# Kernel optimization log

Hardware: AMD Instinct MI355X
Metric: run time of the kernel (lower is better)

Reference implementation:

```python
import jax, jax.numpy as jnp
import numpy as np

NUM_EMBEDDINGS = 1024
EMBEDDING_DIM = 64
BETA = 0.25


def setup_inputs() -> dict:
    key = jax.random.key(0)
    k1, k2 = jax.random.split(key)
    z = jax.random.normal(k1, (16, EMBEDDING_DIM, 64, 64), dtype=jnp.float32)
    # matches torch init: uniform_(-1/K, 1/K)
    lim = 1.0 / NUM_EMBEDDINGS
    embedding = jax.random.uniform(k2, (NUM_EMBEDDINGS, EMBEDDING_DIM),
                                   dtype=jnp.float32, minval=-lim, maxval=lim)
    return {"z": z, "embedding": embedding}


def reference(z, embedding):
    B, C, H, W = z.shape  # C == EMBEDDING_DIM
    # [B,C,H,W] -> [B*H*W, C]
    z_flat = jnp.transpose(z, (0, 2, 3, 1)).reshape(-1, C)
    # squared euclidean distances (argmin-equivalent to torch.cdist):
    # ||z||^2 - 2 z.e + ||e||^2 ; shape [N, K]
    d = (jnp.sum(z_flat * z_flat, axis=-1, keepdims=True)
         - 2.0 * (z_flat @ embedding.T)
         + jnp.sum(embedding * embedding, axis=-1))
    encoding_indices = jnp.argmin(d, axis=1)  # [N] int
    z_q_flat = embedding[encoding_indices]    # gather [N, C]
    z_q = jnp.transpose(z_q_flat.reshape(B, H, W, C), (0, 3, 1, 2))
    vq_loss = jnp.mean(jnp.square(jax.lax.stop_gradient(z_q) - z))
    commitment_loss = BETA * jnp.mean(jnp.square(jax.lax.stop_gradient(z) - z_q))
    return (z_q, encoding_indices, vq_loss + commitment_loss)
```

## Files before the change

kernel.cpp:

```cpp
#include <hip/hip_runtime.h>

#define N_PIX   65536
#define CDIM    64
#define KCODES  1024
#define HWSZ    4096
#define KCHUNK  128
#define NCHUNK  8
#define TPB     256
#define PXT     2

#define OFF_NE   0
#define OFF_MIN  1024
#define OFF_IDX  525312
#define OFF_LOSS 1049600

#define OUT_IDX  (N_PIX * CDIM)
#define OUT_LOSS (OUT_IDX + N_PIX)

__global__ void vq_prep(const float* __restrict__ emb, float* __restrict__ ws) {
#pragma clang fp contract(off)
    int k = blockIdx.x * blockDim.x + threadIdx.x;
    if (k == 0) ws[OFF_LOSS] = 0.0f;
    if (k >= KCODES) return;
    const float* e = emb + k * CDIM;
    float r0 = e[0]*e[0], r1 = e[1]*e[1], r2 = e[2]*e[2], r3 = e[3]*e[3];
    float r4 = e[4]*e[4], r5 = e[5]*e[5], r6 = e[6]*e[6], r7 = e[7]*e[7];
    for (int i = 8; i < CDIM; i += 8) {
        r0 = r0 + e[i+0]*e[i+0]; r1 = r1 + e[i+1]*e[i+1];
        r2 = r2 + e[i+2]*e[i+2]; r3 = r3 + e[i+3]*e[i+3];
        r4 = r4 + e[i+4]*e[i+4]; r5 = r5 + e[i+5]*e[i+5];
        r6 = r6 + e[i+6]*e[i+6]; r7 = r7 + e[i+7]*e[i+7];
    }
    ws[OFF_NE + k] = ((r0 + r1) + (r2 + r3)) + ((r4 + r5) + (r6 + r7));
}

__device__ __forceinline__ float np_nz(const float* zr) {
    float r0 = zr[0]*zr[0], r1 = zr[1]*zr[1], r2 = zr[2]*zr[2], r3 = zr[3]*zr[3];
    float r4 = zr[4]*zr[4], r5 = zr[5]*zr[5], r6 = zr[6]*zr[6], r7 = zr[7]*zr[7];
#pragma unroll
    for (int i = 8; i < CDIM; i += 8) {
        r0 = r0 + zr[i+0]*zr[i+0]; r1 = r1 + zr[i+1]*zr[i+1];
        r2 = r2 + zr[i+2]*zr[i+2]; r3 = r3 + zr[i+3]*zr[i+3];
        r4 = r4 + zr[i+4]*zr[i+4]; r5 = r5 + zr[i+5]*zr[i+5];
        r6 = r6 + zr[i+6]*zr[i+6]; r7 = r7 + zr[i+7]*zr[i+7];
    }
    return ((r0 + r1) + (r2 + r3)) + ((r4 + r5) + (r6 + r7));
}

__global__ __launch_bounds__(TPB, 2) void vq_argmin(const float* __restrict__ z,
                                                    const float* __restrict__ ws,
                                                    const float* __restrict__ emb,
                                                    float* __restrict__ cmin,
                                                    int* __restrict__ cidx) {
#pragma clang fp contract(off)
    __shared__ float se[KCHUNK * CDIM];
    __shared__ float sn[KCHUNK];

    const int chunk = blockIdx.y;
    const int k0 = chunk * KCHUNK;

    const float4* esrc = (const float4*)(emb + (size_t)k0 * CDIM);
    float4* edst = (float4*)se;
    for (int i = threadIdx.x; i < KCHUNK * CDIM / 4; i += TPB) edst[i] = esrc[i];
    for (int i = threadIdx.x; i < KCHUNK; i += TPB) sn[i] = ws[OFF_NE + k0 + i];
    __syncthreads();

    const int p0 = blockIdx.x * (TPB * PXT) + threadIdx.x;
    const int p1 = p0 + TPB;

    float zr0[CDIM], zr1[CDIM];
    {
        const int b0  = p0 >> 12, hw0 = p0 & (HWSZ - 1);
        const int b1  = p1 >> 12, hw1 = p1 & (HWSZ - 1);
        const float* zp0 = z + ((size_t)(b0 * CDIM) << 12) + hw0;
        const float* zp1 = z + ((size_t)(b1 * CDIM) << 12) + hw1;
#pragma unroll
        for (int c = 0; c < CDIM; ++c) {
            zr0[c] = zp0[(size_t)c << 12];
            zr1[c] = zp1[(size_t)c << 12];
        }
    }
    const float nz0 = np_nz(zr0);
    const float nz1 = np_nz(zr1);

    float best0 = 3.4e38f, best1 = 3.4e38f;
    int   bi0   = k0,      bi1   = k0;
    for (int kk = 0; kk < KCHUNK; kk += 2) {
        const float4* e0 = (const float4*)(se + kk * CDIM);
        const float4* e1 = e0 + (CDIM / 4);
        float a00 = 0.f, a01 = 0.f, a10 = 0.f, a11 = 0.f;
#pragma unroll
        for (int j = 0; j < 16; ++j) {
            float4 v0 = e0[j];
            float4 v1 = e1[j];
            a00 = fmaf(zr0[4*j+0], v0.x, a00);
            a00 = fmaf(zr0[4*j+1], v0.y, a00);
            a00 = fmaf(zr0[4*j+2], v0.z, a00);
            a00 = fmaf(zr0[4*j+3], v0.w, a00);
            a01 = fmaf(zr0[4*j+0], v1.x, a01);
            a01 = fmaf(zr0[4*j+1], v1.y, a01);
            a01 = fmaf(zr0[4*j+2], v1.z, a01);
            a01 = fmaf(zr0[4*j+3], v1.w, a01);
            a10 = fmaf(zr1[4*j+0], v0.x, a10);
            a10 = fmaf(zr1[4*j+1], v0.y, a10);
            a10 = fmaf(zr1[4*j+2], v0.z, a10);
            a10 = fmaf(zr1[4*j+3], v0.w, a10);
            a11 = fmaf(zr1[4*j+0], v1.x, a11);
            a11 = fmaf(zr1[4*j+1], v1.y, a11);
            a11 = fmaf(zr1[4*j+2], v1.z, a11);
            a11 = fmaf(zr1[4*j+3], v1.w, a11);
        }
        float d00 = (nz0 - 2.0f * a00) + sn[kk];
        float d01 = (nz0 - 2.0f * a01) + sn[kk + 1];
        float d10 = (nz1 - 2.0f * a10) + sn[kk];
        float d11 = (nz1 - 2.0f * a11) + sn[kk + 1];
        if (d00 < best0) { best0 = d00; bi0 = k0 + kk; }
        if (d01 < best0) { best0 = d01; bi0 = k0 + kk + 1; }
        if (d10 < best1) { best1 = d10; bi1 = k0 + kk; }
        if (d11 < best1) { best1 = d11; bi1 = k0 + kk + 1; }
    }
    cmin[(p0 << 3) + chunk] = best0;
    cidx[(p0 << 3) + chunk] = bi0;
    cmin[(p1 << 3) + chunk] = best1;
    cidx[(p1 << 3) + chunk] = bi1;
}

__global__ __launch_bounds__(TPB) void vq_finalize(const float* __restrict__ z,
                                                   const float* __restrict__ emb,
                                                   const float* __restrict__ cmin,
                                                   const int* __restrict__ cidx,
                                                   float* __restrict__ out,
                                                   float* __restrict__ loss_acc) {
    const int p = blockIdx.x * TPB + threadIdx.x;

    float best = cmin[p << 3];
    int   bi   = cidx[p << 3];
#pragma unroll
    for (int ch = 1; ch < NCHUNK; ++ch) {
        float m = cmin[(p << 3) + ch];
        if (m < best) { best = m; bi = cidx[(p << 3) + ch]; }
    }

    out[OUT_IDX + p] = (float)bi;

    const float* ev = emb + bi * CDIM;
    const int b  = p >> 12;
    const int hw = p & (HWSZ - 1);
    const float* zp = z + ((size_t)(b * CDIM) << 12) + hw;
    float* zq = out + ((size_t)(b * CDIM) << 12) + hw;

    float ls = 0.0f;
#pragma unroll
    for (int c = 0; c < CDIM; ++c) {
        float e = ev[c];
        float zv = zp[(size_t)c << 12];
        float d = e - zv;
        ls = fmaf(d, d, ls);
        zq[(size_t)c << 12] = e;
    }

#pragma unroll
    for (int off = 32; off > 0; off >>= 1) ls += __shfl_down(ls, off);
    __shared__ float wsum[TPB / 64];
    if ((threadIdx.x & 63) == 0) wsum[threadIdx.x >> 6] = ls;
    __syncthreads();
    if (threadIdx.x == 0) {
        float s = wsum[0] + wsum[1] + wsum[2] + wsum[3];
        atomicAdd(loss_acc, s);
    }
}

__global__ void vq_loss_out(const float* __restrict__ loss_acc, float* __restrict__ out) {
    out[OUT_LOSS] = loss_acc[0] * (1.25f / (float)(N_PIX * CDIM));
}

extern "C" void kernel_launch(void* const* d_in, const int* in_sizes, int n_in,
                              void* d_out, int out_size, void* d_ws, size_t ws_size,
                              hipStream_t stream) {
    const float* z   = (const float*)d_in[0];
    const float* emb = (const float*)d_in[1];
    float* ws   = (float*)d_ws;
    float* out  = (float*)d_out;
    float* cmin = ws + OFF_MIN;
    int*   cidx = (int*)(ws + OFF_IDX);
    float* lossp = ws + OFF_LOSS;

    vq_prep<<<dim3(KCODES / TPB), dim3(TPB), 0, stream>>>(emb, ws);
    vq_argmin<<<dim3(N_PIX / (TPB * PXT), NCHUNK), dim3(TPB), 0, stream>>>(z, ws, emb, cmin, cidx);
    vq_finalize<<<dim3(N_PIX / TPB), dim3(TPB), 0, stream>>>(z, emb, cmin, cidx, out, lossp);
    vq_loss_out<<<1, 1, 0, stream>>>(lossp, out);
}
```

Measured before the change: 197.2 us.

## Fuse prep and loss-out kernels, raise pixels per thread to four

Removes the separate codebook-norm prep kernel by computing norms in shared memory inside each argmin block. It also removes the final single-thread loss kernel by having the last finalize block, found through an atomic counter, write the scaled loss. Each thread now handles four pixels instead of two, halving the grid and doubling embedding reuse from shared memory, with launch bounds relaxed to one block per SIMD. The costs are much higher register pressure (256 z values per thread), which risks spills and lower occupancy, and fewer blocks (512) for the GPU's CUs.

Measured after the change: 304.3 us. +54.3%, slower.

```diff
diff --git a/kernel.cpp b/kernel.cpp
--- a/kernel.cpp
+++ b/kernel.cpp
@@ -7,32 +7,16 @@
 #define KCHUNK  128
 #define NCHUNK  8
 #define TPB     256
-#define PXT     2
-
-#define OFF_NE   0
+#define PXT     4
+#define GRIDX   (N_PIX / (TPB * PXT))
+
+#define OFF_CTR  0
 #define OFF_MIN  1024
 #define OFF_IDX  525312
 #define OFF_LOSS 1049600
 
 #define OUT_IDX  (N_PIX * CDIM)
 #define OUT_LOSS (OUT_IDX + N_PIX)
-
-__global__ void vq_prep(const float* __restrict__ emb, float* __restrict__ ws) {
-#pragma clang fp contract(off)
-    int k = blockIdx.x * blockDim.x + threadIdx.x;
-    if (k == 0) ws[OFF_LOSS] = 0.0f;
-    if (k >= KCODES) return;
-    const float* e = emb + k * CDIM;
-    float r0 = e[0]*e[0], r1 = e[1]*e[1], r2 = e[2]*e[2], r3 = e[3]*e[3];
-    float r4 = e[4]*e[4], r5 = e[5]*e[5], r6 = e[6]*e[6], r7 = e[7]*e[7];
-    for (int i = 8; i < CDIM; i += 8) {
-        r0 = r0 + e[i+0]*e[i+0]; r1 = r1 + e[i+1]*e[i+1];
-        r2 = r2 + e[i+2]*e[i+2]; r3 = r3 + e[i+3]*e[i+3];
-        r4 = r4 + e[i+4]*e[i+4]; r5 = r5 + e[i+5]*e[i+5];
-        r6 = r6 + e[i+6]*e[i+6]; r7 = r7 + e[i+7]*e[i+7];
-    }
-    ws[OFF_NE + k] = ((r0 + r1) + (r2 + r3)) + ((r4 + r5) + (r6 + r7));
-}
 
 __device__ __forceinline__ float np_nz(const float* zr) {
     float r0 = zr[0]*zr[0], r1 = zr[1]*zr[1], r2 = zr[2]*zr[2], r3 = zr[3]*zr[3];
@@ -47,11 +31,11 @@
     return ((r0 + r1) + (r2 + r3)) + ((r4 + r5) + (r6 + r7));
 }
 
-__global__ __launch_bounds__(TPB, 2) void vq_argmin(const float* __restrict__ z,
-                                                    const float* __restrict__ ws,
+__global__ __launch_bounds__(TPB, 1) void vq_argmin(const float* __restrict__ z,
                                                     const float* __restrict__ emb,
                                                     float* __restrict__ cmin,
-                                                    int* __restrict__ cidx) {
+                                                    int* __restrict__ cidx,
+                                                    float* __restrict__ ws) {
 #pragma clang fp contract(off)
     __shared__ float se[KCHUNK * CDIM];
     __shared__ float sn[KCHUNK];
@@ -59,36 +43,65 @@
     const int chunk = blockIdx.y;
     const int k0 = chunk * KCHUNK;
 
+    if ((blockIdx.x | blockIdx.y) == 0 && threadIdx.x == 0) {
+        ws[OFF_LOSS] = 0.0f;
+        ((unsigned*)ws)[OFF_CTR] = 0u;
+    }
+
     const float4* esrc = (const float4*)(emb + (size_t)k0 * CDIM);
     float4* edst = (float4*)se;
     for (int i = threadIdx.x; i < KCHUNK * CDIM / 4; i += TPB) edst[i] = esrc[i];
-    for (int i = threadIdx.x; i < KCHUNK; i += TPB) sn[i] = ws[OFF_NE + k0 + i];
+    __syncthreads();
+    if (threadIdx.x < KCHUNK) {
+        const float* e = se + threadIdx.x * CDIM;
+        float r0 = e[0]*e[0], r1 = e[1]*e[1], r2 = e[2]*e[2], r3 = e[3]*e[3];
+        float r4 = e[4]*e[4], r5 = e[5]*e[5], r6 = e[6]*e[6], r7 = e[7]*e[7];
+#pragma unroll
+        for (int i = 8; i < CDIM; i += 8) {
+            r0 = r0 + e[i+0]*e[i+0]; r1 = r1 + e[i+1]*e[i+1];
+            r2 = r2 + e[i+2]*e[i+2]; r3 = r3 + e[i+3]*e[i+3];
+            r4 = r4 + e[i+4]*e[i+4]; r5 = r5 + e[i+5]*e[i+5];
+            r6 = r6 + e[i+6]*e[i+6]; r7 = r7 + e[i+7]*e[i+7];
+        }
+        sn[threadIdx.x] = ((r0 + r1) + (r2 + r3)) + ((r4 + r5) + (r6 + r7));
+    }
     __syncthreads();
 
     const int p0 = blockIdx.x * (TPB * PXT) + threadIdx.x;
     const int p1 = p0 + TPB;
-
-    float zr0[CDIM], zr1[CDIM];
+    const int p2 = p1 + TPB;
+    const int p3 = p2 + TPB;
+
+    float zr0[CDIM], zr1[CDIM], zr2[CDIM], zr3[CDIM];
     {
-        const int b0  = p0 >> 12, hw0 = p0 & (HWSZ - 1);
-        const int b1  = p1 >> 12, hw1 = p1 & (HWSZ - 1);
+        const int b0 = p0 >> 12, hw0 = p0 & (HWSZ - 1);
+        const int b1 = p1 >> 12, hw1 = p1 & (HWSZ - 1);
+        const int b2 = p2 >> 12, hw2 = p2 & (HWSZ - 1);
+        const int b3 = p3 >> 12, hw3 = p3 & (HWSZ - 1);
         const float* zp0 = z + ((size_t)(b0 * CDIM) << 12) + hw0;
         const float* zp1 = z + ((size_t)(b1 * CDIM) << 12) + hw1;
+        const float* zp2 = z + ((size_t)(b2 * CDIM) << 12) + hw2;
+        const float* zp3 = z + ((size_t)(b3 * CDIM) << 12) + hw3;
 #pragma unroll
         for (int c = 0; c < CDIM; ++c) {
             zr0[c] = zp0[(size_t)c << 12];
             zr1[c] = zp1[(size_t)c << 12];
+            zr2[c] = zp2[(size_t)c << 12];
+            zr3[c] = zp3[(size_t)c << 12];
         }
     }
     const float nz0 = np_nz(zr0);
     const float nz1 = np_nz(zr1);
-
-    float best0 = 3.4e38f, best1 = 3.4e38f;
-    int   bi0   = k0,      bi1   = k0;
+    const float nz2 = np_nz(zr2);
+    const float nz3 = np_nz(zr3);
+
+    float best0 = 3.4e38f, best1 = 3.4e38f, best2 = 3.4e38f, best3 = 3.4e38f;
+    int   bi0   = k0,      bi1   = k0,      bi2   = k0,      bi3   = k0;
     for (int kk = 0; kk < KCHUNK; kk += 2) {
         const float4* e0 = (const float4*)(se + kk * CDIM);
         const float4* e1 = e0 + (CDIM / 4);
         float a00 = 0.f, a01 = 0.f, a10 = 0.f, a11 = 0.f;
+        float a20 = 0.f, a21 = 0.f, a30 = 0.f, a31 = 0.f;
 #pragma unroll
         for (int j = 0; j < 16; ++j) {
             float4 v0 = e0[j];
@@ -109,20 +122,48 @@
             a11 = fmaf(zr1[4*j+1], v1.y, a11);
             a11 = fmaf(zr1[4*j+2], v1.z, a11);
             a11 = fmaf(zr1[4*j+3], v1.w, a11);
+            a20 = fmaf(zr2[4*j+0], v0.x, a20);
+            a20 = fmaf(zr2[4*j+1], v0.y, a20);
+            a20 = fmaf(zr2[4*j+2], v0.z, a20);
+            a20 = fmaf(zr2[4*j+3], v0.w, a20);
+            a21 = fmaf(zr2[4*j+0], v1.x, a21);
+            a21 = fmaf(zr2[4*j+1], v1.y, a21);
+            a21 = fmaf(zr2[4*j+2], v1.z, a21);
+            a21 = fmaf(zr2[4*j+3], v1.w, a21);
+            a30 = fmaf(zr3[4*j+0], v0.x, a30);
+            a30 = fmaf(zr3[4*j+1], v0.y, a30);
+            a30 = fmaf(zr3[4*j+2], v0.z, a30);
+            a30 = fmaf(zr3[4*j+3], v0.w, a30);
+            a31 = fmaf(zr3[4*j+0], v1.x, a31);
+            a31 = fmaf(zr3[4*j+1], v1.y, a31);
+            a31 = fmaf(zr3[4*j+2], v1.z, a31);
+            a31 = fmaf(zr3[4*j+3], v1.w, a31);
         }
         float d00 = (nz0 - 2.0f * a00) + sn[kk];
         float d01 = (nz0 - 2.0f * a01) + sn[kk + 1];
         float d10 = (nz1 - 2.0f * a10) + sn[kk];
         float d11 = (nz1 - 2.0f * a11) + sn[kk + 1];
+        float d20 = (nz2 - 2.0f * a20) + sn[kk];
+        float d21 = (nz2 - 2.0f * a21) + sn[kk + 1];
+        float d30 = (nz3 - 2.0f * a30) + sn[kk];
+        float d31 = (nz3 - 2.0f * a31) + sn[kk + 1];
         if (d00 < best0) { best0 = d00; bi0 = k0 + kk; }
         if (d01 < best0) { best0 = d01; bi0 = k0 + kk + 1; }
         if (d10 < best1) { best1 = d10; bi1 = k0 + kk; }
         if (d11 < best1) { best1 = d11; bi1 = k0 + kk + 1; }
+        if (d20 < best2) { best2 = d20; bi2 = k0 + kk; }
+        if (d21 < best2) { best2 = d21; bi2 = k0 + kk + 1; }
+        if (d30 < best3) { best3 = d30; bi3 = k0 + kk; }
+        if (d31 < best3) { best3 = d31; bi3 = k0 + kk + 1; }
     }
     cmin[(p0 << 3) + chunk] = best0;
     cidx[(p0 << 3) + chunk] = bi0;
     cmin[(p1 << 3) + chunk] = best1;
     cidx[(p1 << 3) + chunk] = bi1;
+    cmin[(p2 << 3) + chunk] = best2;
+    cidx[(p2 << 3) + chunk] = bi2;
+    cmin[(p3 << 3) + chunk] = best3;
+    cidx[(p3 << 3) + chunk] = bi3;
 }
 
 __global__ __launch_bounds__(TPB) void vq_finalize(const float* __restrict__ z,
@@ -130,7 +171,7 @@
                                                    const float* __restrict__ cmin,
                                                    const int* __restrict__ cidx,
                                                    float* __restrict__ out,
-                                                   float* __restrict__ loss_acc) {
+                                                   float* __restrict__ ws) {
     const int p = blockIdx.x * TPB + threadIdx.x;
 
     float best = cmin[p << 3];
@@ -166,12 +207,17 @@
     __syncthreads();
     if (threadIdx.x == 0) {
         float s = wsum[0] + wsum[1] + wsum[2] + wsum[3];
+        float* loss_acc = ws + OFF_LOSS;
         atomicAdd(loss_acc, s);
-    }
-}
-
-__global__ void vq_loss_out(const float* __restrict__ loss_acc, float* __restrict__ out) {
-    out[OUT_LOSS] = loss_acc[0] * (1.25f / (float)(N_PIX * CDIM));
+        __threadfence();
+        unsigned* ctr = (unsigned*)ws + OFF_CTR;
+        unsigned old = atomicAdd(ctr, 1u);
+        if (old == (unsigned)(gridDim.x - 1)) {
+            __threadfence();
+            float total = atomicAdd(loss_acc, 0.0f);
+            out[OUT_LOSS] = total * (1.25f / (float)(N_PIX * CDIM));
+        }
+    }
 }
 
 extern "C" void kernel_launch(void* const* d_in, const int* in_sizes, int n_in,
@@ -183,10 +229,7 @@
     float* out  = (float*)d_out;
     float* cmin = ws + OFF_MIN;
     int*   cidx = (int*)(ws + OFF_IDX);
-    float* lossp = ws + OFF_LOSS;
-
-    vq_prep<<<dim3(KCODES / TPB), dim3(TPB), 0, stream>>>(emb, ws);
-    vq_argmin<<<dim3(N_PIX / (TPB * PXT), NCHUNK), dim3(TPB), 0, stream>>>(z, ws, emb, cmin, cidx);
-    vq_finalize<<<dim3(N_PIX / TPB), dim3(TPB), 0, stream>>>(z, emb, cmin, cidx, out, lossp);
-    vq_loss_out<<<1, 1, 0, stream>>>(lossp, out);
-}
+
+    vq_argmin<<<dim3(GRIDX, NCHUNK), dim3(TPB), 0, stream>>>(z, emb, cmin, cidx, ws);
+    vq_finalize<<<dim3(N_PIX / TPB), dim3(TPB), 0, stream>>>(z, emb, cmin, cidx, out, ws);
+}
```

## Fuse codebook-norm prep and loss finalization into argmin and finalize kernels

Applied to the files above, without the earlier changes.

Removes the separate prep kernel by computing codebook squared norms per block from the shared-memory chunk. It also drops the single-thread loss output kernel, replacing it with a last-block-done counter in the finalize kernel. This cuts two launches and their gaps, at the cost of redundant norm work per block and an extra syncthreads. Launch bounds are raised from 2 to 3 blocks per CU, which may force register spills in the argmin kernel because each thread holds 128 z values in registers.

Result: no change. 200.2 us (+1.5%).

```diff
diff --git a/kernel.cpp b/kernel.cpp
--- a/kernel.cpp
+++ b/kernel.cpp
@@ -8,31 +8,15 @@
 #define NCHUNK  8
 #define TPB     256
 #define PXT     2
+#define GRIDX   (N_PIX / (TPB * PXT))
 
-#define OFF_NE   0
+#define OFF_CTR  0
 #define OFF_MIN  1024
 #define OFF_IDX  525312
 #define OFF_LOSS 1049600
 
 #define OUT_IDX  (N_PIX * CDIM)
 #define OUT_LOSS (OUT_IDX + N_PIX)
-
-__global__ void vq_prep(const float* __restrict__ emb, float* __restrict__ ws) {
-#pragma clang fp contract(off)
-    int k = blockIdx.x * blockDim.x + threadIdx.x;
-    if (k == 0) ws[OFF_LOSS] = 0.0f;
-    if (k >= KCODES) return;
-    const float* e = emb + k * CDIM;
-    float r0 = e[0]*e[0], r1 = e[1]*e[1], r2 = e[2]*e[2], r3 = e[3]*e[3];
-    float r4 = e[4]*e[4], r5 = e[5]*e[5], r6 = e[6]*e[6], r7 = e[7]*e[7];
-    for (int i = 8; i < CDIM; i += 8) {
-        r0 = r0 + e[i+0]*e[i+0]; r1 = r1 + e[i+1]*e[i+1];
-        r2 = r2 + e[i+2]*e[i+2]; r3 = r3 + e[i+3]*e[i+3];
-        r4 = r4 + e[i+4]*e[i+4]; r5 = r5 + e[i+5]*e[i+5];
-        r6 = r6 + e[i+6]*e[i+6]; r7 = r7 + e[i+7]*e[i+7];
-    }
-    ws[OFF_NE + k] = ((r0 + r1) + (r2 + r3)) + ((r4 + r5) + (r6 + r7));
-}
 
 __device__ __forceinline__ float np_nz(const float* zr) {
     float r0 = zr[0]*zr[0], r1 = zr[1]*zr[1], r2 = zr[2]*zr[2], r3 = zr[3]*zr[3];
@@ -47,11 +31,11 @@
     return ((r0 + r1) + (r2 + r3)) + ((r4 + r5) + (r6 + r7));
 }
 
-__global__ __launch_bounds__(TPB, 2) void vq_argmin(const float* __restrict__ z,
-                                                    const float* __restrict__ ws,
+__global__ __launch_bounds__(TPB, 3) void vq_argmin(const float* __restrict__ z,
                                                     const float* __restrict__ emb,
                                                     float* __restrict__ cmin,
-                                                    int* __restrict__ cidx) {
+                                                    int* __restrict__ cidx,
+                                                    float* __restrict__ ws) {
 #pragma clang fp contract(off)
     __shared__ float se[KCHUNK * CDIM];
     __shared__ float sn[KCHUNK];
@@ -59,10 +43,28 @@
     const int chunk = blockIdx.y;
     const int k0 = chunk * KCHUNK;
 
+    if ((blockIdx.x | blockIdx.y) == 0 && threadIdx.x == 0) {
+        ws[OFF_LOSS] = 0.0f;
+        ((unsigned*)ws)[OFF_CTR] = 0u;
+    }
+
     const float4* esrc = (const float4*)(emb + (size_t)k0 * CDIM);
     float4* edst = (float4*)se;
     for (int i = threadIdx.x; i < KCHUNK * CDIM / 4; i += TPB) edst[i] = esrc[i];
-    for (int i = threadIdx.x; i < KCHUNK; i += TPB) sn[i] = ws[OFF_NE + k0 + i];
+    __syncthreads();
+    if (threadIdx.x < KCHUNK) {
+        const float* e = se + threadIdx.x * CDIM;
+        float r0 = e[0]*e[0], r1 = e[1]*e[1], r2 = e[2]*e[2], r3 = e[3]*e[3];
+        float r4 = e[4]*e[4], r5 = e[5]*e[5], r6 = e[6]*e[6], r7 = e[7]*e[7];
+#pragma unroll
+        for (int i = 8; i < CDIM; i += 8) {
+            r0 = r0 + e[i+0]*e[i+0]; r1 = r1 + e[i+1]*e[i+1];
+            r2 = r2 + e[i+2]*e[i+2]; r3 = r3 + e[i+3]*e[i+3];
+            r4 = r4 + e[i+4]*e[i+4]; r5 = r5 + e[i+5]*e[i+5];
+            r6 = r6 + e[i+6]*e[i+6]; r7 = r7 + e[i+7]*e[i+7];
+        }
+        sn[threadIdx.x] = ((r0 + r1) + (r2 + r3)) + ((r4 + r5) + (r6 + r7));
+    }
     __syncthreads();
 
     const int p0 = blockIdx.x * (TPB * PXT) + threadIdx.x;
@@ -130,7 +132,7 @@
                                                    const float* __restrict__ cmin,
                                                    const int* __restrict__ cidx,
                                                    float* __restrict__ out,
-                                                   float* __restrict__ loss_acc) {
+                                                   float* __restrict__ ws) {
     const int p = blockIdx.x * TPB + threadIdx.x;
 
     float best = cmin[p << 3];
@@ -166,12 +168,17 @@
     __syncthreads();
     if (threadIdx.x == 0) {
         float s = wsum[0] + wsum[1] + wsum[2] + wsum[3];
+        float* loss_acc = ws + OFF_LOSS;
         atomicAdd(loss_acc, s);
+        __threadfence();
+        unsigned* ctr = (unsigned*)ws + OFF_CTR;
+        unsigned old = atomicAdd(ctr, 1u);
+        if (old == (unsigned)(gridDim.x - 1)) {
+            __threadfence();
+            float total = atomicAdd(loss_acc, 0.0f);
+            out[OUT_LOSS] = total * (1.25f / (float)(N_PIX * CDIM));
+        }
     }
-}
-
-__global__ void vq_loss_out(const float* __restrict__ loss_acc, float* __restrict__ out) {
-    out[OUT_LOSS] = loss_acc[0] * (1.25f / (float)(N_PIX * CDIM));
 }
 
 extern "C" void kernel_launch(void* const* d_in, const int* in_sizes, int n_in,
@@ -183,10 +190,7 @@
     float* out  = (float*)d_out;
     float* cmin = ws + OFF_MIN;
     int*   cidx = (int*)(ws + OFF_IDX);
-    float* lossp = ws + OFF_LOSS;
 
-    vq_prep<<<dim3(KCODES / TPB), dim3(TPB), 0, stream>>>(emb, ws);
-    vq_argmin<<<dim3(N_PIX / (TPB * PXT), NCHUNK), dim3(TPB), 0, stream>>>(z, ws, emb, cmin, cidx);
-    vq_finalize<<<dim3(N_PIX / TPB), dim3(TPB), 0, stream>>>(z, emb, cmin, cidx, out, lossp);
-    vq_loss_out<<<1, 1, 0, stream>>>(lossp, out);
+    vq_argmin<<<dim3(GRIDX, NCHUNK), dim3(TPB), 0, stream>>>(z, emb, cmin, cidx, ws);
+    vq_finalize<<<dim3(N_PIX / TPB), dim3(TPB), 0, stream>>>(z, emb, cmin, cidx, out, ws);
 }
```

## Load codebook rows via scalar loads instead of LDS staging in argmin

Applied to the files above, without the earlier changes.

Drops the shared-memory staging of the codebook chunk in the argmin kernel and reads each pair of codebook rows straight from global memory with inline-asm scalar loads (s_load_dwordx16) into SGPRs. The FMAs then take wave-uniform scalar operands, removing LDS reads and the block barrier. Launch bounds rise to three blocks per SIMD slot to raise occupancy. The trade is a large SGPR footprint (about 128 SGPRs for codebook data per iteration) and s_waitcnt stalls on scalar-cache latency with no prefetch overlap. The tighter launch bounds may also force spills of the 128-float z register arrays.

Result: no change. 199.7 us (+1.3%).

```diff
diff --git a/kernel.cpp b/kernel.cpp
--- a/kernel.cpp
+++ b/kernel.cpp
@@ -8,6 +8,7 @@
 #define NCHUNK  8
 #define TPB     256
 #define PXT     2
+#define GRIDX   (N_PIX / (TPB * PXT))
 
 #define OFF_NE   0
 #define OFF_MIN  1024
@@ -16,6 +17,9 @@
 
 #define OUT_IDX  (N_PIX * CDIM)
 #define OUT_LOSS (OUT_IDX + N_PIX)
+
+typedef __attribute__((ext_vector_type(16))) float f32x16;
+typedef __attribute__((ext_vector_type(2)))  float f32x2;
 
 __global__ void vq_prep(const float* __restrict__ emb, float* __restrict__ ws) {
 #pragma clang fp contract(off)
@@ -47,23 +51,14 @@
     return ((r0 + r1) + (r2 + r3)) + ((r4 + r5) + (r6 + r7));
 }
 
-__global__ __launch_bounds__(TPB, 2) void vq_argmin(const float* __restrict__ z,
+__global__ __launch_bounds__(TPB, 3) void vq_argmin(const float* __restrict__ z,
                                                     const float* __restrict__ ws,
                                                     const float* __restrict__ emb,
                                                     float* __restrict__ cmin,
                                                     int* __restrict__ cidx) {
 #pragma clang fp contract(off)
-    __shared__ float se[KCHUNK * CDIM];
-    __shared__ float sn[KCHUNK];
-
     const int chunk = blockIdx.y;
     const int k0 = chunk * KCHUNK;
-
-    const float4* esrc = (const float4*)(emb + (size_t)k0 * CDIM);
-    float4* edst = (float4*)se;
-    for (int i = threadIdx.x; i < KCHUNK * CDIM / 4; i += TPB) edst[i] = esrc[i];
-    for (int i = threadIdx.x; i < KCHUNK; i += TPB) sn[i] = ws[OFF_NE + k0 + i];
-    __syncthreads();
 
     const int p0 = blockIdx.x * (TPB * PXT) + threadIdx.x;
     const int p1 = p0 + TPB;
@@ -85,35 +80,69 @@
 
     float best0 = 3.4e38f, best1 = 3.4e38f;
     int   bi0   = k0,      bi1   = k0;
+
+    const float* wsne = ws + OFF_NE + k0;
+
     for (int kk = 0; kk < KCHUNK; kk += 2) {
-        const float4* e0 = (const float4*)(se + kk * CDIM);
-        const float4* e1 = e0 + (CDIM / 4);
+        const float* erow = emb + (size_t)(k0 + kk) * CDIM;
+        const float* snp  = wsne + kk;
+
         float a00 = 0.f, a01 = 0.f, a10 = 0.f, a11 = 0.f;
-#pragma unroll
-        for (int j = 0; j < 16; ++j) {
-            float4 v0 = e0[j];
-            float4 v1 = e1[j];
-            a00 = fmaf(zr0[4*j+0], v0.x, a00);
-            a00 = fmaf(zr0[4*j+1], v0.y, a00);
-            a00 = fmaf(zr0[4*j+2], v0.z, a00);
-            a00 = fmaf(zr0[4*j+3], v0.w, a00);
-            a01 = fmaf(zr0[4*j+0], v1.x, a01);
-            a01 = fmaf(zr0[4*j+1], v1.y, a01);
-            a01 = fmaf(zr0[4*j+2], v1.z, a01);
-            a01 = fmaf(zr0[4*j+3], v1.w, a01);
-            a10 = fmaf(zr1[4*j+0], v0.x, a10);
-            a10 = fmaf(zr1[4*j+1], v0.y, a10);
-            a10 = fmaf(zr1[4*j+2], v0.z, a10);
-            a10 = fmaf(zr1[4*j+3], v0.w, a10);
-            a11 = fmaf(zr1[4*j+0], v1.x, a11);
-            a11 = fmaf(zr1[4*j+1], v1.y, a11);
-            a11 = fmaf(zr1[4*j+2], v1.z, a11);
-            a11 = fmaf(zr1[4*j+3], v1.w, a11);
-        }
-        float d00 = (nz0 - 2.0f * a00) + sn[kk];
-        float d01 = (nz0 - 2.0f * a01) + sn[kk + 1];
-        float d10 = (nz1 - 2.0f * a10) + sn[kk];
-        float d11 = (nz1 - 2.0f * a11) + sn[kk + 1];
+
+        f32x16 ea0, ea1, eb0, eb1;
+        f32x2  snv;
+        asm volatile(
+            "s_load_dwordx16 %0, %5, 0x0\n\t"
+            "s_load_dwordx16 %1, %5, 0x40\n\t"
+            "s_load_dwordx16 %2, %5, 0x100\n\t"
+            "s_load_dwordx16 %3, %5, 0x140\n\t"
+            "s_load_dwordx2  %4, %6, 0x0\n\t"
+            "s_waitcnt lgkmcnt(0)"
+            : "=s"(ea0), "=s"(ea1), "=s"(eb0), "=s"(eb1), "=s"(snv)
+            : "s"(erow), "s"(snp));
+#pragma unroll
+        for (int j = 0; j < 16; ++j) {
+            a00 = fmaf(zr0[j], ea0[j], a00);
+            a01 = fmaf(zr0[j], eb0[j], a01);
+            a10 = fmaf(zr1[j], ea0[j], a10);
+            a11 = fmaf(zr1[j], eb0[j], a11);
+        }
+#pragma unroll
+        for (int j = 0; j < 16; ++j) {
+            a00 = fmaf(zr0[16+j], ea1[j], a00);
+            a01 = fmaf(zr0[16+j], eb1[j], a01);
+            a10 = fmaf(zr1[16+j], ea1[j], a10);
+            a11 = fmaf(zr1[16+j], eb1[j], a11);
+        }
+
+        f32x16 ec0, ec1, ed0, ed1;
+        asm volatile(
+            "s_load_dwordx16 %0, %4, 0x80\n\t"
+            "s_load_dwordx16 %1, %4, 0xc0\n\t"
+            "s_load_dwordx16 %2, %4, 0x180\n\t"
+            "s_load_dwordx16 %3, %4, 0x1c0\n\t"
+            "s_waitcnt lgkmcnt(0)"
+            : "=s"(ec0), "=s"(ec1), "=s"(ed0), "=s"(ed1)
+            : "s"(erow));
+#pragma unroll
+        for (int j = 0; j < 16; ++j) {
+            a00 = fmaf(zr0[32+j], ec0[j], a00);
+            a01 = fmaf(zr0[32+j], ed0[j], a01);
+            a10 = fmaf(zr1[32+j], ec0[j], a10);
+            a11 = fmaf(zr1[32+j], ed0[j], a11);
+        }
+#pragma unroll
+        for (int j = 0; j < 16; ++j) {
+            a00 = fmaf(zr0[48+j], ec1[j], a00);
+            a01 = fmaf(zr0[48+j], ed1[j], a01);
+            a10 = fmaf(zr1[48+j], ec1[j], a10);
+            a11 = fmaf(zr1[48+j], ed1[j], a11);
+        }
+
+        float d00 = (nz0 - 2.0f * a00) + snv[0];
+        float d01 = (nz0 - 2.0f * a01) + snv[1];
+        float d10 = (nz1 - 2.0f * a10) + snv[0];
+        float d11 = (nz1 - 2.0f * a11) + snv[1];
         if (d00 < best0) { best0 = d00; bi0 = k0 + kk; }
         if (d01 < best0) { best0 = d01; bi0 = k0 + kk + 1; }
         if (d10 < best1) { best1 = d10; bi1 = k0 + kk; }
@@ -186,7 +215,7 @@
     float* lossp = ws + OFF_LOSS;
 
     vq_prep<<<dim3(KCODES / TPB), dim3(TPB), 0, stream>>>(emb, ws);
-    vq_argmin<<<dim3(N_PIX / (TPB * PXT), NCHUNK), dim3(TPB), 0, stream>>>(z, ws, emb, cmin, cidx);
+    vq_argmin<<<dim3(GRIDX, NCHUNK), dim3(TPB), 0, stream>>>(z, ws, emb, cmin, cidx);
     vq_finalize<<<dim3(N_PIX / TPB), dim3(TPB), 0, stream>>>(z, emb, cmin, cidx, out, lossp);
     vq_loss_out<<<1, 1, 0, stream>>>(lossp, out);
 }
```
